# Kernel tuning notes

Measured on AMD Instinct MI355X. Metric: run time of the kernel, lower is better.

Reference implementation:

```python
import jax, jax.numpy as jnp
import numpy as np

B, S, D_IN, D_OUT = 4, 2048, 2048, 2048
E, R = 8, 8
SCALING = 16.0 / 8.0  # lora_alpha / r
# Dropout (p=0.05) treated as identity (eval mode) for a deterministic reference.

def setup_inputs() -> dict:
    key = jax.random.key(0)
    ks = jax.random.split(key, 8)
    x = jax.random.normal(ks[0], (B, S, D_IN), dtype=jnp.float32)
    base_W = jax.random.normal(ks[1], (D_OUT, D_IN), dtype=jnp.float32) * 0.02
    base_b = jax.random.normal(ks[2], (D_OUT,), dtype=jnp.float32) * 0.02
    shared_A = jax.random.normal(ks[3], (R, D_IN), dtype=jnp.float32) * 0.01
    shared_B = jax.random.normal(ks[4], (D_OUT, R), dtype=jnp.float32) * 0.01
    expert_A = jax.random.normal(ks[5], (E, R, D_IN), dtype=jnp.float32) * 0.01
    expert_B = jax.random.normal(ks[6], (E, D_OUT, R), dtype=jnp.float32) * 0.01
    task_emb = jax.random.normal(ks[7], (E, D_IN), dtype=jnp.float32) * 0.01
    collab_w = jnp.array(0.5, dtype=jnp.float32)
    return {"x": x, "base_W": base_W, "base_b": base_b,
            "shared_A": shared_A, "shared_B": shared_B,
            "expert_A": expert_A, "expert_B": expert_B,
            "task_emb": task_emb, "collab_w": collab_w}

def reference(x, base_W, base_b, shared_A, shared_B, expert_A, expert_B, task_emb, collab_w):
    # base linear: [B,S,D_out]
    base_out = jnp.einsum('bsi,oi->bso', x, base_W) + base_b
    # shared LoRA path
    shared_out = jnp.einsum('bsr,or->bso', jnp.einsum('bsi,ri->bsr', x, shared_A), shared_B) * SCALING
    # soft routing over task experts (task_id=None branch)
    x_mean = x.mean(axis=1)                               # [B,D_in]
    routing = jax.nn.softmax(x_mean @ task_emb.T, axis=-1)  # [B,E]
    t = jnp.einsum('bsi,eri->bser', x, expert_A)          # [B,S,E,R] low-rank
    task_out = jnp.einsum('bser,eor,be->bso', t, expert_B, routing) * SCALING
    cw = jax.nn.sigmoid(collab_w)
    return base_out + cw * shared_out + (1.0 - cw) * task_out
```

## Files before the change

### kernel.cpp

```cpp
#include <hip/hip_runtime.h>
#include <hip/hip_bf16.h>
#include <math.h>

#define BATCH 4
#define SEQ   2048
#define DIN   2048
#define DOUT  2048
#define NEXP  8
#define RANK  8
#define MTOT  (BATCH * SEQ)
#define KP    128

typedef __bf16 bf16x8 __attribute__((ext_vector_type(8)));
typedef __bf16 bf16x4 __attribute__((ext_vector_type(4)));
typedef float  f32x4  __attribute__((ext_vector_type(4)));

#define GLOBAL_AS __attribute__((address_space(1)))
#define LDS_AS    __attribute__((address_space(3)))

__global__ __launch_bounds__(256) void prep_all(
    const float* __restrict__ x, const float* __restrict__ W,
    const float* __restrict__ expert_A, const float* __restrict__ shared_A,
    const float* __restrict__ expert_B, const float* __restrict__ shared_B,
    const float* __restrict__ collab,
    __bf16* __restrict__ xb, float* __restrict__ x_mean,
    __bf16* __restrict__ Wb, __bf16* __restrict__ caug, __bf16* __restrict__ Ab)
{
    const int bid = blockIdx.x;
    const int t = threadIdx.x;
    if (bid < 256) {
        const int dc = bid & 1, sc = (bid >> 1) & 31, b = bid >> 6;
        const int i = dc * 1024 + t * 4;
        size_t base = ((size_t)b * SEQ + (size_t)sc * 64) * DIN + i;
        float ax = 0.f, ay = 0.f, az = 0.f, aw = 0.f;
        for (int s = 0; s < 64; ++s) {
            float4 v = *(const float4*)&x[base + (size_t)s * DIN];
            ax += v.x; ay += v.y; az += v.z; aw += v.w;
            bf16x4 h = { (__bf16)v.x, (__bf16)v.y, (__bf16)v.z, (__bf16)v.w };
            *(bf16x4*)&xb[base + (size_t)s * DIN] = h;
        }
        atomicAdd(&x_mean[(size_t)b * DIN + i],     ax);
        atomicAdd(&x_mean[(size_t)b * DIN + i + 1], ay);
        atomicAdd(&x_mean[(size_t)b * DIN + i + 2], az);
        atomicAdd(&x_mean[(size_t)b * DIN + i + 3], aw);
    } else if (bid < 4352) {
        size_t idx = ((size_t)(bid - 256) * 256 + t) * 4;
        float4 v = *(const float4*)&W[idx];
        bf16x4 h = { (__bf16)v.x, (__bf16)v.y, (__bf16)v.z, (__bf16)v.w };
        *(bf16x4*)&Wb[idx] = h;
    } else if (bid < 5376) {
        int idx = (bid - 4352) * 256 + t;
        int k = idx & 127, o = idx >> 7;
        float cw = 1.0f / (1.0f + expf(-collab[0]));
        float v = 0.f;
        if (k < 64)
            v = (1.0f - cw) * 2.0f * expert_B[((size_t)(k >> 3) * DOUT + o) * RANK + (k & 7)];
        else if (k < 72)
            v = cw * 2.0f * shared_B[(size_t)o * RANK + (k - 64)];
        caug[idx] = (__bf16)v;
    } else {
        int idx = (bid - 5376) * 256 + t;
        int i = idx & 2047, k = idx >> 11;
        float v = 0.f;
        if (k < 64)      v = expert_A[(size_t)k * DIN + i];
        else if (k < 72) v = shared_A[(size_t)(k - 64) * DIN + i];
        Ab[idx] = (__bf16)v;
    }
}

__global__ __launch_bounds__(256) void gemm_t_rout(
    const __bf16* __restrict__ xb, const __bf16* __restrict__ Ab,
    const float* __restrict__ x_mean, const float* __restrict__ task_emb,
    __bf16* __restrict__ pt, float* __restrict__ routing)
{
    __shared__ __bf16 lsA[128 * 32];
    __shared__ __bf16 lsB[128 * 32];
    __shared__ float red[256];
    __shared__ float logits[NEXP];
    const int bid = blockIdx.x;
    const int t = threadIdx.x;

    if (bid >= 256) {
        const int b = bid - 256;
        float le[NEXP] = {0.f,0.f,0.f,0.f,0.f,0.f,0.f,0.f};
        for (int j = 0; j < DIN / 256; ++j) {
            int i = t + j * 256;
            float xm = x_mean[(size_t)b * DIN + i] * (1.0f / (float)SEQ);
            #pragma unroll
            for (int e = 0; e < NEXP; ++e)
                le[e] += xm * task_emb[(size_t)e * DIN + i];
        }
        for (int e = 0; e < NEXP; ++e) {
            red[t] = le[e];
            __syncthreads();
            for (int s = 128; s > 0; s >>= 1) {
                if (t < s) red[t] += red[t + s];
                __syncthreads();
            }
            if (t == 0) logits[e] = red[0];
            __syncthreads();
        }
        if (t == 0) {
            float mx = logits[0];
            for (int e = 1; e < NEXP; ++e) mx = fmaxf(mx, logits[e]);
            float ex[NEXP], den = 0.f;
            for (int e = 0; e < NEXP; ++e) { ex[e] = expf(logits[e] - mx); den += ex[e]; }
            for (int e = 0; e < NEXP; ++e) routing[b * NEXP + e] = ex[e] / den;
        }
        return;
    }

    const int lane = t & 63;
    const int wm = (t >> 6) >> 1, wn = (t >> 6) & 1;
    const int kc = bid & 3;
    const int m0 = (bid >> 2) * 128;

    f32x4 acc[4][4];
    #pragma unroll
    for (int a = 0; a < 4; ++a)
        #pragma unroll
        for (int c = 0; c < 4; ++c) acc[a][c] = (f32x4){0.f, 0.f, 0.f, 0.f};

    for (int k0 = kc * 512; k0 < kc * 512 + 512; k0 += 32) {
        #pragma unroll
        for (int q = 0; q < 2; ++q) {
            int L = q * 256 + t;
            int row = L >> 2, seg = L & 3;
            const __bf16* gpA = xb + (size_t)(m0 + row) * DIN + k0 + seg * 8;
            const __bf16* gpB = Ab + (size_t)row * DIN + k0 + seg * 8;
            int Lu = q * 256 + (t & ~63);
            __builtin_amdgcn_global_load_lds((GLOBAL_AS void*)gpA,
                (LDS_AS void*)&lsA[Lu * 8], 16, 0, 0);
            __builtin_amdgcn_global_load_lds((GLOBAL_AS void*)gpB,
                (LDS_AS void*)&lsB[Lu * 8], 16, 0, 0);
        }
        __syncthreads();
        bf16x8 af[4], bfr[4];
        #pragma unroll
        for (int tm = 0; tm < 4; ++tm)
            af[tm]  = *(const bf16x8*)&lsA[(wm * 64 + tm * 16 + (lane & 15)) * 32 + (lane >> 4) * 8];
        #pragma unroll
        for (int tn = 0; tn < 4; ++tn)
            bfr[tn] = *(const bf16x8*)&lsB[(wn * 64 + tn * 16 + (lane & 15)) * 32 + (lane >> 4) * 8];
        #pragma unroll
        for (int tm = 0; tm < 4; ++tm)
            #pragma unroll
            for (int tn = 0; tn < 4; ++tn)
                acc[tm][tn] = __builtin_amdgcn_mfma_f32_16x16x32_bf16(
                    af[tm], bfr[tn], acc[tm][tn], 0, 0, 0);
        __syncthreads();
    }
    #pragma unroll
    for (int tm = 0; tm < 4; ++tm)
        #pragma unroll
        for (int tn = 0; tn < 4; ++tn) {
            int col = wn * 64 + tn * 16 + (lane & 15);
            #pragma unroll
            for (int v = 0; v < 4; ++v) {
                int row = m0 + wm * 64 + tm * 16 + (lane >> 4) * 4 + v;
                pt[((size_t)kc * MTOT + row) * KP + col] = (__bf16)acc[tm][tn][v];
            }
        }
}

__global__ __launch_bounds__(256) void reduce_route(
    const __bf16* __restrict__ pt, const float* __restrict__ routing,
    __bf16* __restrict__ tb)
{
    size_t idx = ((size_t)blockIdx.x * 256 + threadIdx.x) * 4;
    int k0 = (int)(idx & 127);
    int m  = (int)(idx >> 7);
    int b  = m >> 11;
    float f = (k0 < 64) ? routing[b * NEXP + (k0 >> 3)] : 1.0f;
    float sx = 0.f, sy = 0.f, sz = 0.f, sw = 0.f;
    #pragma unroll
    for (int kc = 0; kc < 4; ++kc) {
        bf16x4 v = *(const bf16x4*)&pt[(size_t)kc * MTOT * KP + idx];
        sx += (float)v[0]; sy += (float)v[1]; sz += (float)v[2]; sw += (float)v[3];
    }
    bf16x4 h = { (__bf16)(sx * f), (__bf16)(sy * f), (__bf16)(sz * f), (__bf16)(sw * f) };
    *(bf16x4*)&tb[idx] = h;
}

__global__ __launch_bounds__(256) void gemm_main(
    const __bf16* __restrict__ xb, const __bf16* __restrict__ Wb,
    const __bf16* __restrict__ tb, const __bf16* __restrict__ caug,
    const float* __restrict__ bias, float* __restrict__ out)
{
    __shared__ __bf16 lsA[128 * 64];
    __shared__ __bf16 lsB[128 * 64];
    const int t = threadIdx.x;
    const int lane = t & 63;
    const int wm = (t >> 6) >> 1, wn = (t >> 6) & 1;
    const int m0 = blockIdx.x * 128;
    const int n0 = blockIdx.y * 128;

    f32x4 acc[4][4];
    #pragma unroll
    for (int a = 0; a < 4; ++a)
        #pragma unroll
        for (int c = 0; c < 4; ++c) acc[a][c] = (f32x4){0.f, 0.f, 0.f, 0.f};

    auto kstep = [&](const __bf16* baseA, const __bf16* baseB,
                     int strideA, int strideB, int k0) {
        #pragma unroll
        for (int q = 0; q < 4; ++q) {
            int G = q * 256 + t;
            int row = G >> 3, sl = G & 7;
            int seg = sl ^ (row & 7);
            const __bf16* gpA = baseA + (size_t)row * strideA + k0 + seg * 8;
            const __bf16* gpB = baseB + (size_t)row * strideB + k0 + seg * 8;
            int Lu = (q * 256 + (t & ~63)) * 8;
            __builtin_amdgcn_global_load_lds((GLOBAL_AS void*)gpA,
                (LDS_AS void*)&lsA[Lu], 16, 0, 0);
            __builtin_amdgcn_global_load_lds((GLOBAL_AS void*)gpB,
                (LDS_AS void*)&lsB[Lu], 16, 0, 0);
        }
        __syncthreads();
        #pragma unroll
        for (int kk = 0; kk < 2; ++kk) {
            bf16x8 af[4], bfr[4];
            #pragma unroll
            for (int tm = 0; tm < 4; ++tm) {
                int r = wm * 64 + tm * 16 + (lane & 15);
                int slot = (kk * 4 + (lane >> 4)) ^ (r & 7);
                af[tm] = *(const bf16x8*)&lsA[r * 64 + slot * 8];
            }
            #pragma unroll
            for (int tn = 0; tn < 4; ++tn) {
                int r = wn * 64 + tn * 16 + (lane & 15);
                int slot = (kk * 4 + (lane >> 4)) ^ (r & 7);
                bfr[tn] = *(const bf16x8*)&lsB[r * 64 + slot * 8];
            }
            #pragma unroll
            for (int tm = 0; tm < 4; ++tm)
                #pragma unroll
                for (int tn = 0; tn < 4; ++tn)
                    acc[tm][tn] = __builtin_amdgcn_mfma_f32_16x16x32_bf16(
                        af[tm], bfr[tn], acc[tm][tn], 0, 0, 0);
        }
        __syncthreads();
    };

    for (int k0 = 0; k0 < DIN; k0 += 64)
        kstep(xb + (size_t)m0 * DIN, Wb + (size_t)n0 * DIN, DIN, DIN, k0);
    for (int k0 = 0; k0 < KP; k0 += 64)
        kstep(tb + (size_t)m0 * KP, caug + (size_t)n0 * KP, KP, KP, k0);

    #pragma unroll
    for (int tm = 0; tm < 4; ++tm)
        #pragma unroll
        for (int tn = 0; tn < 4; ++tn) {
            int col = n0 + wn * 64 + tn * 16 + (lane & 15);
            float bv = bias[col];
            #pragma unroll
            for (int v = 0; v < 4; ++v) {
                int row = m0 + wm * 64 + tm * 16 + (lane >> 4) * 4 + v;
                out[(size_t)row * DOUT + col] = acc[tm][tn][v] + bv;
            }
        }
}

extern "C" void kernel_launch(void* const* d_in, const int* in_sizes, int n_in,
                              void* d_out, int out_size, void* d_ws, size_t ws_size,
                              hipStream_t stream)
{
    const float* x        = (const float*)d_in[0];
    const float* base_W   = (const float*)d_in[1];
    const float* base_b   = (const float*)d_in[2];
    const float* shared_A = (const float*)d_in[3];
    const float* shared_B = (const float*)d_in[4];
    const float* expert_A = (const float*)d_in[5];
    const float* expert_B = (const float*)d_in[6];
    const float* task_emb = (const float*)d_in[7];
    const float* collab_w = (const float*)d_in[8];
    float* out = (float*)d_out;

    char* ws = (char*)d_ws;
    __bf16* xb      = (__bf16*)(ws + 0);
    __bf16* Wb      = (__bf16*)(ws + 33554432);
    __bf16* pt      = (__bf16*)(ws + 41943040);
    __bf16* tb      = (__bf16*)(ws + 50331648);
    __bf16* caug    = (__bf16*)(ws + 52428800);
    __bf16* Ab      = (__bf16*)(ws + 52953088);
    float*  x_mean  = (float*) (ws + 53477376);
    float*  routing = (float*) (ws + 53510144);

    hipMemsetAsync(x_mean, 0, BATCH * DIN * sizeof(float), stream);
    prep_all    <<<dim3(6400), 256, 0, stream>>>(x, base_W, expert_A, shared_A,
                                                 expert_B, shared_B, collab_w,
                                                 xb, x_mean, Wb, caug, Ab);
    gemm_t_rout <<<dim3(260), 256, 0, stream>>>(xb, Ab, x_mean, task_emb, pt, routing);
    reduce_route<<<dim3(1024), 256, 0, stream>>>(pt, routing, tb);
    gemm_main   <<<dim3(64, 16), 256, 0, stream>>>(xb, Wb, tb, caug, base_b, out);
}
```

Before: 245.3 us.

## Fuse routing softmax and split-K reduction into low-rank GEMM, drop atomics

Replaces the atomic x_mean accumulation with per-chunk partial sums that each low-rank GEMM block reduces itself, then computes the routing softmax in-block. The low-rank projection now runs the full K per block and applies the routing scale in its epilogue, which removes the split-K partial buffer, the reduce kernel, the memset and one launch. The cost is that only 64 blocks run the 2048-deep low-rank GEMM with no split-K parallelism, and every block redundantly re-reduces partials and recomputes the softmax. The main GEMM also precomputes its global and LDS address offsets outside the loop.

```diff
diff --git a/kernel.cpp b/kernel.cpp
--- a/kernel.cpp
+++ b/kernel.cpp
@@ -23,7 +23,7 @@
     const float* __restrict__ expert_A, const float* __restrict__ shared_A,
     const float* __restrict__ expert_B, const float* __restrict__ shared_B,
     const float* __restrict__ collab,
-    __bf16* __restrict__ xb, float* __restrict__ x_mean,
+    __bf16* __restrict__ xb, float* __restrict__ partial,
     __bf16* __restrict__ Wb, __bf16* __restrict__ caug, __bf16* __restrict__ Ab)
 {
     const int bid = blockIdx.x;
@@ -39,10 +39,8 @@
             bf16x4 h = { (__bf16)v.x, (__bf16)v.y, (__bf16)v.z, (__bf16)v.w };
             *(bf16x4*)&xb[base + (size_t)s * DIN] = h;
         }
-        atomicAdd(&x_mean[(size_t)b * DIN + i],     ax);
-        atomicAdd(&x_mean[(size_t)b * DIN + i + 1], ay);
-        atomicAdd(&x_mean[(size_t)b * DIN + i + 2], az);
-        atomicAdd(&x_mean[(size_t)b * DIN + i + 3], aw);
+        float4 p = { ax, ay, az, aw };
+        *(float4*)&partial[((size_t)b * 32 + sc) * DIN + i] = p;
     } else if (bid < 4352) {
         size_t idx = ((size_t)(bid - 256) * 256 + t) * 4;
         float4 v = *(const float4*)&W[idx];
@@ -68,60 +66,61 @@
     }
 }
 
-__global__ __launch_bounds__(256) void gemm_t_rout(
+__global__ __launch_bounds__(256) void gemm_t64(
     const __bf16* __restrict__ xb, const __bf16* __restrict__ Ab,
-    const float* __restrict__ x_mean, const float* __restrict__ task_emb,
-    __bf16* __restrict__ pt, float* __restrict__ routing)
+    const float* __restrict__ partial, const float* __restrict__ task_emb,
+    __bf16* __restrict__ tb)
 {
     __shared__ __bf16 lsA[128 * 32];
     __shared__ __bf16 lsB[128 * 32];
     __shared__ float red[256];
-    __shared__ float logits[NEXP];
-    const int bid = blockIdx.x;
+    __shared__ float rs[NEXP];
     const int t = threadIdx.x;
-
-    if (bid >= 256) {
-        const int b = bid - 256;
-        float le[NEXP] = {0.f,0.f,0.f,0.f,0.f,0.f,0.f,0.f};
-        for (int j = 0; j < DIN / 256; ++j) {
-            int i = t + j * 256;
-            float xm = x_mean[(size_t)b * DIN + i] * (1.0f / (float)SEQ);
-            #pragma unroll
-            for (int e = 0; e < NEXP; ++e)
-                le[e] += xm * task_emb[(size_t)e * DIN + i];
-        }
-        for (int e = 0; e < NEXP; ++e) {
-            red[t] = le[e];
+    const int m0 = blockIdx.x * 128;
+    const int b  = m0 >> 11;
+
+    float xm[8] = {0.f,0.f,0.f,0.f,0.f,0.f,0.f,0.f};
+    for (int sc = 0; sc < 32; ++sc) {
+        const float* pp = partial + ((size_t)b * 32 + sc) * DIN + t * 8;
+        float4 v0 = *(const float4*)pp, v1 = *(const float4*)(pp + 4);
+        xm[0] += v0.x; xm[1] += v0.y; xm[2] += v0.z; xm[3] += v0.w;
+        xm[4] += v1.x; xm[5] += v1.y; xm[6] += v1.z; xm[7] += v1.w;
+    }
+    float le[NEXP];
+    #pragma unroll
+    for (int e = 0; e < NEXP; ++e) {
+        const float* te = task_emb + (size_t)e * DIN + t * 8;
+        float4 u0 = *(const float4*)te, u1 = *(const float4*)(te + 4);
+        le[e] = xm[0]*u0.x + xm[1]*u0.y + xm[2]*u0.z + xm[3]*u0.w
+              + xm[4]*u1.x + xm[5]*u1.y + xm[6]*u1.z + xm[7]*u1.w;
+    }
+    for (int e = 0; e < NEXP; ++e) {
+        red[t] = le[e];
+        __syncthreads();
+        for (int s = 128; s > 0; s >>= 1) {
+            if (t < s) red[t] += red[t + s];
             __syncthreads();
-            for (int s = 128; s > 0; s >>= 1) {
-                if (t < s) red[t] += red[t + s];
-                __syncthreads();
-            }
-            if (t == 0) logits[e] = red[0];
-            __syncthreads();
-        }
-        if (t == 0) {
-            float mx = logits[0];
-            for (int e = 1; e < NEXP; ++e) mx = fmaxf(mx, logits[e]);
-            float ex[NEXP], den = 0.f;
-            for (int e = 0; e < NEXP; ++e) { ex[e] = expf(logits[e] - mx); den += ex[e]; }
-            for (int e = 0; e < NEXP; ++e) routing[b * NEXP + e] = ex[e] / den;
-        }
-        return;
+        }
+        if (t == 0) rs[e] = red[0] * (1.0f / (float)SEQ);
+        __syncthreads();
+    }
+    if (t == 0) {
+        float mx = rs[0];
+        for (int e = 1; e < NEXP; ++e) mx = fmaxf(mx, rs[e]);
+        float ex[NEXP], den = 0.f;
+        for (int e = 0; e < NEXP; ++e) { ex[e] = expf(rs[e] - mx); den += ex[e]; }
+        for (int e = 0; e < NEXP; ++e) rs[e] = ex[e] / den;
     }
 
     const int lane = t & 63;
     const int wm = (t >> 6) >> 1, wn = (t >> 6) & 1;
-    const int kc = bid & 3;
-    const int m0 = (bid >> 2) * 128;
-
     f32x4 acc[4][4];
     #pragma unroll
     for (int a = 0; a < 4; ++a)
         #pragma unroll
         for (int c = 0; c < 4; ++c) acc[a][c] = (f32x4){0.f, 0.f, 0.f, 0.f};
 
-    for (int k0 = kc * 512; k0 < kc * 512 + 512; k0 += 32) {
+    for (int k0 = 0; k0 < DIN; k0 += 32) {
         #pragma unroll
         for (int q = 0; q < 2; ++q) {
             int L = q * 256 + t;
@@ -150,36 +149,19 @@
                     af[tm], bfr[tn], acc[tm][tn], 0, 0, 0);
         __syncthreads();
     }
+
     #pragma unroll
     for (int tm = 0; tm < 4; ++tm)
         #pragma unroll
         for (int tn = 0; tn < 4; ++tn) {
             int col = wn * 64 + tn * 16 + (lane & 15);
+            float f = (col < 64) ? rs[col >> 3] : 1.0f;
             #pragma unroll
             for (int v = 0; v < 4; ++v) {
                 int row = m0 + wm * 64 + tm * 16 + (lane >> 4) * 4 + v;
-                pt[((size_t)kc * MTOT + row) * KP + col] = (__bf16)acc[tm][tn][v];
+                tb[(size_t)row * KP + col] = (__bf16)(acc[tm][tn][v] * f);
             }
         }
-}
-
-__global__ __launch_bounds__(256) void reduce_route(
-    const __bf16* __restrict__ pt, const float* __restrict__ routing,
-    __bf16* __restrict__ tb)
-{
-    size_t idx = ((size_t)blockIdx.x * 256 + threadIdx.x) * 4;
-    int k0 = (int)(idx & 127);
-    int m  = (int)(idx >> 7);
-    int b  = m >> 11;
-    float f = (k0 < 64) ? routing[b * NEXP + (k0 >> 3)] : 1.0f;
-    float sx = 0.f, sy = 0.f, sz = 0.f, sw = 0.f;
-    #pragma unroll
-    for (int kc = 0; kc < 4; ++kc) {
-        bf16x4 v = *(const bf16x4*)&pt[(size_t)kc * MTOT * KP + idx];
-        sx += (float)v[0]; sy += (float)v[1]; sz += (float)v[2]; sw += (float)v[3];
-    }
-    bf16x4 h = { (__bf16)(sx * f), (__bf16)(sy * f), (__bf16)(sz * f), (__bf16)(sw * f) };
-    *(bf16x4*)&tb[idx] = h;
 }
 
 __global__ __launch_bounds__(256) void gemm_main(
@@ -195,43 +177,58 @@
     const int m0 = blockIdx.x * 128;
     const int n0 = blockIdx.y * 128;
 
+    int rowq[4], segq[4], ldso[4];
+    #pragma unroll
+    for (int q = 0; q < 4; ++q) {
+        rowq[q] = q * 32 + (t >> 3);
+        segq[q] = (t & 7) ^ (rowq[q] & 7);
+        ldso[q] = (q * 256 + (t & ~63)) * 8;
+    }
+    const __bf16* pA[4]; const __bf16* pB[4];
+    #pragma unroll
+    for (int q = 0; q < 4; ++q) {
+        pA[q] = xb + (size_t)(m0 + rowq[q]) * DIN + segq[q] * 8;
+        pB[q] = Wb + (size_t)(n0 + rowq[q]) * DIN + segq[q] * 8;
+    }
+    int aoff[2][4], boff[2][4];
+    #pragma unroll
+    for (int tm = 0; tm < 4; ++tm) {
+        int r = wm * 64 + tm * 16 + (lane & 15);
+        #pragma unroll
+        for (int kk = 0; kk < 2; ++kk)
+            aoff[kk][tm] = r * 64 + (((kk * 4 + (lane >> 4)) ^ (r & 7)) * 8);
+    }
+    #pragma unroll
+    for (int tn = 0; tn < 4; ++tn) {
+        int r = wn * 64 + tn * 16 + (lane & 15);
+        #pragma unroll
+        for (int kk = 0; kk < 2; ++kk)
+            boff[kk][tn] = r * 64 + (((kk * 4 + (lane >> 4)) ^ (r & 7)) * 8);
+    }
+
     f32x4 acc[4][4];
     #pragma unroll
     for (int a = 0; a < 4; ++a)
         #pragma unroll
         for (int c = 0; c < 4; ++c) acc[a][c] = (f32x4){0.f, 0.f, 0.f, 0.f};
 
-    auto kstep = [&](const __bf16* baseA, const __bf16* baseB,
-                     int strideA, int strideB, int k0) {
+    for (int it = 0; it < 32; ++it) {
         #pragma unroll
         for (int q = 0; q < 4; ++q) {
-            int G = q * 256 + t;
-            int row = G >> 3, sl = G & 7;
-            int seg = sl ^ (row & 7);
-            const __bf16* gpA = baseA + (size_t)row * strideA + k0 + seg * 8;
-            const __bf16* gpB = baseB + (size_t)row * strideB + k0 + seg * 8;
-            int Lu = (q * 256 + (t & ~63)) * 8;
-            __builtin_amdgcn_global_load_lds((GLOBAL_AS void*)gpA,
-                (LDS_AS void*)&lsA[Lu], 16, 0, 0);
-            __builtin_amdgcn_global_load_lds((GLOBAL_AS void*)gpB,
-                (LDS_AS void*)&lsB[Lu], 16, 0, 0);
+            __builtin_amdgcn_global_load_lds((GLOBAL_AS void*)pA[q],
+                (LDS_AS void*)&lsA[ldso[q]], 16, 0, 0);
+            __builtin_amdgcn_global_load_lds((GLOBAL_AS void*)pB[q],
+                (LDS_AS void*)&lsB[ldso[q]], 16, 0, 0);
+            pA[q] += 64; pB[q] += 64;
         }
         __syncthreads();
         #pragma unroll
         for (int kk = 0; kk < 2; ++kk) {
             bf16x8 af[4], bfr[4];
             #pragma unroll
-            for (int tm = 0; tm < 4; ++tm) {
-                int r = wm * 64 + tm * 16 + (lane & 15);
-                int slot = (kk * 4 + (lane >> 4)) ^ (r & 7);
-                af[tm] = *(const bf16x8*)&lsA[r * 64 + slot * 8];
-            }
-            #pragma unroll
-            for (int tn = 0; tn < 4; ++tn) {
-                int r = wn * 64 + tn * 16 + (lane & 15);
-                int slot = (kk * 4 + (lane >> 4)) ^ (r & 7);
-                bfr[tn] = *(const bf16x8*)&lsB[r * 64 + slot * 8];
-            }
+            for (int tm = 0; tm < 4; ++tm) af[tm]  = *(const bf16x8*)&lsA[aoff[kk][tm]];
+            #pragma unroll
+            for (int tn = 0; tn < 4; ++tn) bfr[tn] = *(const bf16x8*)&lsB[boff[kk][tn]];
             #pragma unroll
             for (int tm = 0; tm < 4; ++tm)
                 #pragma unroll
@@ -240,12 +237,40 @@
                         af[tm], bfr[tn], acc[tm][tn], 0, 0, 0);
         }
         __syncthreads();
-    };
-
-    for (int k0 = 0; k0 < DIN; k0 += 64)
-        kstep(xb + (size_t)m0 * DIN, Wb + (size_t)n0 * DIN, DIN, DIN, k0);
-    for (int k0 = 0; k0 < KP; k0 += 64)
-        kstep(tb + (size_t)m0 * KP, caug + (size_t)n0 * KP, KP, KP, k0);
+    }
+
+    const __bf16* qA[4]; const __bf16* qB[4];
+    #pragma unroll
+    for (int q = 0; q < 4; ++q) {
+        qA[q] = tb   + (size_t)(m0 + rowq[q]) * KP + segq[q] * 8;
+        qB[q] = caug + (size_t)(n0 + rowq[q]) * KP + segq[q] * 8;
+    }
+    for (int it = 0; it < 2; ++it) {
+        #pragma unroll
+        for (int q = 0; q < 4; ++q) {
+            __builtin_amdgcn_global_load_lds((GLOBAL_AS void*)qA[q],
+                (LDS_AS void*)&lsA[ldso[q]], 16, 0, 0);
+            __builtin_amdgcn_global_load_lds((GLOBAL_AS void*)qB[q],
+                (LDS_AS void*)&lsB[ldso[q]], 16, 0, 0);
+            qA[q] += 64; qB[q] += 64;
+        }
+        __syncthreads();
+        #pragma unroll
+        for (int kk = 0; kk < 2; ++kk) {
+            bf16x8 af[4], bfr[4];
+            #pragma unroll
+            for (int tm = 0; tm < 4; ++tm) af[tm]  = *(const bf16x8*)&lsA[aoff[kk][tm]];
+            #pragma unroll
+            for (int tn = 0; tn < 4; ++tn) bfr[tn] = *(const bf16x8*)&lsB[boff[kk][tn]];
+            #pragma unroll
+            for (int tm = 0; tm < 4; ++tm)
+                #pragma unroll
+                for (int tn = 0; tn < 4; ++tn)
+                    acc[tm][tn] = __builtin_amdgcn_mfma_f32_16x16x32_bf16(
+                        af[tm], bfr[tn], acc[tm][tn], 0, 0, 0);
+        }
+        __syncthreads();
+    }
 
     #pragma unroll
     for (int tm = 0; tm < 4; ++tm)
@@ -279,18 +304,14 @@
     char* ws = (char*)d_ws;
     __bf16* xb      = (__bf16*)(ws + 0);
     __bf16* Wb      = (__bf16*)(ws + 33554432);
-    __bf16* pt      = (__bf16*)(ws + 41943040);
-    __bf16* tb      = (__bf16*)(ws + 50331648);
-    __bf16* caug    = (__bf16*)(ws + 52428800);
-    __bf16* Ab      = (__bf16*)(ws + 52953088);
-    float*  x_mean  = (float*) (ws + 53477376);
-    float*  routing = (float*) (ws + 53510144);
-
-    hipMemsetAsync(x_mean, 0, BATCH * DIN * sizeof(float), stream);
-    prep_all    <<<dim3(6400), 256, 0, stream>>>(x, base_W, expert_A, shared_A,
-                                                 expert_B, shared_B, collab_w,
-                                                 xb, x_mean, Wb, caug, Ab);
-    gemm_t_rout <<<dim3(260), 256, 0, stream>>>(xb, Ab, x_mean, task_emb, pt, routing);
-    reduce_route<<<dim3(1024), 256, 0, stream>>>(pt, routing, tb);
-    gemm_main   <<<dim3(64, 16), 256, 0, stream>>>(xb, Wb, tb, caug, base_b, out);
+    __bf16* tb      = (__bf16*)(ws + 41943040);
+    __bf16* caug    = (__bf16*)(ws + 44040192);
+    __bf16* Ab      = (__bf16*)(ws + 44564480);
+    float*  partial = (float*) (ws + 45088768);
+
+    prep_all <<<dim3(6400), 256, 0, stream>>>(x, base_W, expert_A, shared_A,
+                                              expert_B, shared_B, collab_w,
+                                              xb, partial, Wb, caug, Ab);
+    gemm_t64 <<<dim3(64), 256, 0, stream>>>(xb, Ab, partial, task_emb, tb);
+    gemm_main<<<dim3(64, 16), 256, 0, stream>>>(xb, Wb, tb, caug, base_b, out);
 }
```

Result: slower. 260.6 us (+6.3%).
